# Optimization experiments

Measured on AMD Instinct MI355X. Metric: run time of the kernel, lower is better.

Reference implementation:

```python
import jax, jax.numpy as jnp
import numpy as np

SIGMA_POS = 0.5
SIGMA_FEAT = 1.0


def setup_inputs() -> dict:
    key = jax.random.key(0)
    ks = jax.random.split(key, 6)
    B, N, M, D, F = 4, 4096, 4096, 3, 64
    return {
        "pos1": jax.random.normal(ks[0], (B, N, D), dtype=jnp.float32),
        "feat1": jax.random.normal(ks[1], (B, N, F), dtype=jnp.float32),
        "w1": jax.random.uniform(ks[2], (B, N, 1), dtype=jnp.float32),
        "pos2": jax.random.normal(ks[3], (B, M, D), dtype=jnp.float32),
        "feat2": jax.random.normal(ks[4], (B, M, F), dtype=jnp.float32),
        "w2": jax.random.uniform(ks[5], (B, M, 1), dtype=jnp.float32),
    }


def reference(pos1, feat1, w1, pos2, feat2, w2):
    # pairwise squared distances via |a|^2 + |b|^2 - 2 a.b  (avoids B,N,M,D tensor)
    sq1 = jnp.sum(pos1 ** 2, axis=-1)  # (B, N)
    sq2 = jnp.sum(pos2 ** 2, axis=-1)  # (B, M)
    cross = jnp.einsum("bnd,bmd->bnm", pos1, pos2)  # (B, N, M)
    pos_dist_sq = sq1[:, :, None] + sq2[:, None, :] - 2.0 * cross
    pos_kernel = jnp.exp(-pos_dist_sq / (2.0 * SIGMA_POS ** 2))
    feat_inner = jnp.einsum("bnf,bmf->bnm", feat1, feat2)  # (B, N, M)
    feat_kernel = jnp.exp(-feat_inner / (2.0 * SIGMA_FEAT ** 2))
    weight_outer = w1 * jnp.swapaxes(w2, 1, 2)  # (B,N,1)*(B,1,M) -> (B,N,M)
    kernel = jnp.sum(pos_kernel * feat_kernel * weight_outer, axis=(1, 2))  # (B,)
    return kernel
```

## Files before the change

kernel.cpp:

```cpp
#include <hip/hip_runtime.h>
#include <stdint.h>


typedef _Float16 f16;
typedef _Float16 v8h __attribute__((ext_vector_type(8)));
typedef _Float16 h4  __attribute__((ext_vector_type(4)));
typedef float    v4f __attribute__((ext_vector_type(4)));

#define L2E 1.4426950408889634f
#define BN 4096
#define KP 96

__device__ __forceinline__ void load_lds16(const void* g, void* s) {
    __builtin_amdgcn_global_load_lds((const __attribute__((address_space(1))) void*)g,
                                     (__attribute__((address_space(3))) void*)s,
                                     16, 0, 0);
}

__global__ __launch_bounds__(256) void prep_kernel(
    const float* __restrict__ pos1, const float* __restrict__ feat1, const float* __restrict__ w1,
    const float* __restrict__ pos2, const float* __restrict__ feat2, const float* __restrict__ w2,
    f16* __restrict__ U1, f16* __restrict__ U2,
    float* __restrict__ la1, float* __restrict__ la2)
{
    int tid  = threadIdx.x;
    int ridx = blockIdx.x * 16 + (tid >> 4);
    int c    = tid & 15;
    int side = ridx >> 14;
    int idx  = ridx & 16383;

    const float* feat = side ? feat2 : feat1;
    f16* U   = side ? U2 : U1;
    float fs = side ? -0.5f * L2E : 1.0f;

    float4 v = ((const float4*)feat)[idx * 16 + c];
    *(h4*)(U + (long)idx * KP + 4 + c * 4) =
        h4{(f16)(v.x * fs), (f16)(v.y * fs), (f16)(v.z * fs), (f16)(v.w * fs)};

    if (c == 0) {
        const float* pos = side ? pos2 : pos1;
        const float* w   = side ? w2   : w1;
        float* la = side ? la2 : la1;
        float ps  = side ? 2.0f * L2E : 2.0f;
        float p0 = pos[idx*3+0], p1 = pos[idx*3+1], p2 = pos[idx*3+2];
        la[idx] = __builtin_amdgcn_logf(w[idx]) - 2.0f * L2E * (p0*p0 + p1*p1 + p2*p2);
        *(h4*)(U + (long)idx * KP) = h4{(f16)(p0*ps), (f16)(p1*ps), (f16)(p2*ps), (f16)0.0f};
    } else if (c <= 7) {
        *(h4*)(U + (long)idx * KP + 68 + (c - 1) * 4) =
            h4{(f16)0.0f, (f16)0.0f, (f16)0.0f, (f16)0.0f};
    }
}

__global__ __launch_bounds__(512, 4) void varifold_kernel(
    const f16* __restrict__ U1, const f16* __restrict__ U2,
    const float* __restrict__ la1, const float* __restrict__ la2,
    float* __restrict__ pw)
{
    __shared__ __align__(1024) f16 sAB[(128 + 256) * KP];
    __shared__ float s1[128];
    __shared__ float s2[256];
    __shared__ float sred[8];

    f16* sA = sAB;
    f16* sB = sAB + 128 * KP;

    int mb = blockIdx.x, nb = blockIdx.y, b = blockIdx.z;
    int tid = threadIdx.x;
    int wave = tid >> 6, lane = tid & 63;

    const char* gA = (const char*)(U1 + ((long)b*BN + nb*128) * KP);
    const char* gB = (const char*)(U2 + ((long)b*BN + mb*256) * KP);

    #pragma unroll
    for (int i = 0; i < 9; ++i) {
        int c = wave * 9 + i;
        const char* src = (c < 24) ? (gA + c * 1024 + lane * 16)
                                   : (gB + (c - 24) * 1024 + lane * 16);
        load_lds16(src, (char*)sAB + c * 1024);
    }
    if (tid < 128)      s1[tid]       = la1[(long)b*BN + nb*128 + tid];
    else if (tid < 384) s2[tid - 128] = la2[(long)b*BN + mb*256 + (tid - 128)];
    __syncthreads();

    int wr = wave >> 2, wc = wave & 3;
    int l15 = lane & 15, quad = lane >> 4;
    int ko = quad * 8;

    v4f acc[4][4];
    #pragma unroll
    for (int i = 0; i < 4; ++i)
        #pragma unroll
        for (int j = 0; j < 4; ++j)
            acc[i][j] = v4f{0.f, 0.f, 0.f, 0.f};

    const f16* Ab = sA + (wr*64 + l15) * KP + ko;
    const f16* Bb = sB + (wc*64 + l15) * KP + ko;
    #pragma unroll
    for (int kk = 0; kk < KP; kk += 32) {
        v8h af[4], bf[4];
        #pragma unroll
        for (int i = 0; i < 4; ++i) af[i] = *(const v8h*)(Ab + i*16*KP + kk);
        #pragma unroll
        for (int j = 0; j < 4; ++j) bf[j] = *(const v8h*)(Bb + j*16*KP + kk);
        #pragma unroll
        for (int i = 0; i < 4; ++i)
            #pragma unroll
            for (int j = 0; j < 4; ++j)
                acc[i][j] = __builtin_amdgcn_mfma_f32_16x16x32_f16(af[i], bf[j], acc[i][j], 0, 0, 0);
    }

    float psum = 0.f;
    #pragma unroll
    for (int i = 0; i < 4; ++i) {
        float4 l1 = *(const float4*)&s1[wr*64 + i*16 + quad*4];
        #pragma unroll
        for (int j = 0; j < 4; ++j) {
            float l2 = s2[wc*64 + j*16 + l15];
            v4f d = acc[i][j];
            psum += __builtin_amdgcn_exp2f(d[0] + l1.x + l2);
            psum += __builtin_amdgcn_exp2f(d[1] + l1.y + l2);
            psum += __builtin_amdgcn_exp2f(d[2] + l1.z + l2);
            psum += __builtin_amdgcn_exp2f(d[3] + l1.w + l2);
        }
    }

    #pragma unroll
    for (int off = 32; off > 0; off >>= 1) psum += __shfl_down(psum, off);
    if (lane == 0) sred[wave] = psum;
    __syncthreads();
    if (tid == 0) {
        float s = 0.f;
        #pragma unroll
        for (int w = 0; w < 8; ++w) s += sred[w];
        pw[(long)b * 512 + nb * 16 + mb] = s;
    }
}

__global__ __launch_bounds__(256) void reduce_kernel(
    const float* __restrict__ pw, float* __restrict__ out)
{
    __shared__ float sred[4];
    int b = blockIdx.x, tid = threadIdx.x;
    float v = pw[(long)b * 512 + tid] + pw[(long)b * 512 + 256 + tid];
    #pragma unroll
    for (int off = 32; off > 0; off >>= 1) v += __shfl_down(v, off);
    if ((tid & 63) == 0) sred[tid >> 6] = v;
    __syncthreads();
    if (tid == 0) out[b] = sred[0] + sred[1] + sred[2] + sred[3];
}

extern "C" void kernel_launch(void* const* d_in, const int* in_sizes, int n_in,
                              void* d_out, int out_size, void* d_ws, size_t ws_size,
                              hipStream_t stream) {
    const float* pos1  = (const float*)d_in[0];
    const float* feat1 = (const float*)d_in[1];
    const float* w1    = (const float*)d_in[2];
    const float* pos2  = (const float*)d_in[3];
    const float* feat2 = (const float*)d_in[4];
    const float* w2    = (const float*)d_in[5];
    float* out = (float*)d_out;

    char* ws = (char*)d_ws;
    f16*   U1  = (f16*)(ws);
    f16*   U2  = (f16*)(ws + 3145728);
    float* la1 = (float*)(ws + 6291456);
    float* la2 = (float*)(ws + 6291456 + 65536);
    float* pw  = (float*)(ws + 6291456 + 131072);

    prep_kernel<<<2048, 256, 0, stream>>>(pos1, feat1, w1, pos2, feat2, w2, U1, U2, la1, la2);
    dim3 grid(16, 32, 4);
    varifold_kernel<<<grid, 512, 0, stream>>>(U1, U2, la1, la2, pw);
    reduce_kernel<<<4, 256, 0, stream>>>(pw, out);
}
```

Baseline: 94.04 us.

## Replace LDS-tiled GEMM with register-resident B columns and streamed A rows

Drops the shared-memory staging of both tiles. Each wave now keeps its 64 B columns (all K) in registers and streams 16-row A fragments straight from global memory with a one-step prefetch. It loops over 256 rows per block, so the grid and partial-sum layout change and reduce_kernel sums 1024 partials. This removes the LDS loads, the barrier and the 16-accumulator tile, at the cost of repeated global/L2 reads of A across the waves and stripes and less reuse per loaded fragment.

```diff
diff --git a/kernel.cpp b/kernel.cpp
--- a/kernel.cpp
+++ b/kernel.cpp
@@ -10,12 +10,6 @@
 #define L2E 1.4426950408889634f
 #define BN 4096
 #define KP 96
-
-__device__ __forceinline__ void load_lds16(const void* g, void* s) {
-    __builtin_amdgcn_global_load_lds((const __attribute__((address_space(1))) void*)g,
-                                     (__attribute__((address_space(3))) void*)s,
-                                     16, 0, 0);
-}
 
 __global__ __launch_bounds__(256) void prep_kernel(
     const float* __restrict__ pos1, const float* __restrict__ feat1, const float* __restrict__ w1,
@@ -51,89 +45,69 @@
     }
 }
 
-__global__ __launch_bounds__(512, 4) void varifold_kernel(
+__global__ __launch_bounds__(256, 4) void varifold_kernel(
     const f16* __restrict__ U1, const f16* __restrict__ U2,
     const float* __restrict__ la1, const float* __restrict__ la2,
     float* __restrict__ pw)
 {
-    __shared__ __align__(1024) f16 sAB[(128 + 256) * KP];
-    __shared__ float s1[128];
-    __shared__ float s2[256];
-    __shared__ float sred[8];
+    int tid = threadIdx.x, wave = tid >> 6, lane = tid & 63;
+    int stripe = blockIdx.x, nchunk = blockIdx.y, b = blockIdx.z;
+    int l15 = lane & 15, quad = lane >> 4;
 
-    f16* sA = sAB;
-    f16* sB = sAB + 128 * KP;
+    long colr = (long)b*BN + stripe*256 + wave*64;
+    long row0 = (long)b*BN + nchunk*256;
 
-    int mb = blockIdx.x, nb = blockIdx.y, b = blockIdx.z;
-    int tid = threadIdx.x;
-    int wave = tid >> 6, lane = tid & 63;
+    v8h bf[3][4];
+    float la2v[4];
+    #pragma unroll
+    for (int j = 0; j < 4; ++j) {
+        const f16* r = U2 + (colr + j*16 + l15) * KP + quad*8;
+        bf[0][j] = *(const v8h*)(r);
+        bf[1][j] = *(const v8h*)(r + 32);
+        bf[2][j] = *(const v8h*)(r + 64);
+        la2v[j]  = la2[colr + j*16 + l15];
+    }
 
-    const char* gA = (const char*)(U1 + ((long)b*BN + nb*128) * KP);
-    const char* gB = (const char*)(U2 + ((long)b*BN + mb*256) * KP);
+    const f16* Ab = U1 + (row0 + l15) * KP + quad*8;
+    v8h afc[3], afn[3];
+    afc[0] = *(const v8h*)(Ab);
+    afc[1] = *(const v8h*)(Ab + 32);
+    afc[2] = *(const v8h*)(Ab + 64);
 
-    #pragma unroll
-    for (int i = 0; i < 9; ++i) {
-        int c = wave * 9 + i;
-        const char* src = (c < 24) ? (gA + c * 1024 + lane * 16)
-                                   : (gB + (c - 24) * 1024 + lane * 16);
-        load_lds16(src, (char*)sAB + c * 1024);
-    }
-    if (tid < 128)      s1[tid]       = la1[(long)b*BN + nb*128 + tid];
-    else if (tid < 384) s2[tid - 128] = la2[(long)b*BN + mb*256 + (tid - 128)];
-    __syncthreads();
+    float psum = 0.f;
+    #pragma unroll 2
+    for (int t = 0; t < 16; ++t) {
+        const f16* An = Ab + (t < 15 ? (t+1) : t) * 16 * KP;
+        afn[0] = *(const v8h*)(An);
+        afn[1] = *(const v8h*)(An + 32);
+        afn[2] = *(const v8h*)(An + 64);
 
-    int wr = wave >> 2, wc = wave & 3;
-    int l15 = lane & 15, quad = lane >> 4;
-    int ko = quad * 8;
-
-    v4f acc[4][4];
-    #pragma unroll
-    for (int i = 0; i < 4; ++i)
+        v4f acc[4];
         #pragma unroll
-        for (int j = 0; j < 4; ++j)
-            acc[i][j] = v4f{0.f, 0.f, 0.f, 0.f};
-
-    const f16* Ab = sA + (wr*64 + l15) * KP + ko;
-    const f16* Bb = sB + (wc*64 + l15) * KP + ko;
-    #pragma unroll
-    for (int kk = 0; kk < KP; kk += 32) {
-        v8h af[4], bf[4];
+        for (int j = 0; j < 4; ++j) acc[j] = v4f{0.f, 0.f, 0.f, 0.f};
         #pragma unroll
-        for (int i = 0; i < 4; ++i) af[i] = *(const v8h*)(Ab + i*16*KP + kk);
-        #pragma unroll
-        for (int j = 0; j < 4; ++j) bf[j] = *(const v8h*)(Bb + j*16*KP + kk);
-        #pragma unroll
-        for (int i = 0; i < 4; ++i)
+        for (int k = 0; k < 3; ++k)
             #pragma unroll
             for (int j = 0; j < 4; ++j)
-                acc[i][j] = __builtin_amdgcn_mfma_f32_16x16x32_f16(af[i], bf[j], acc[i][j], 0, 0, 0);
-    }
+                acc[j] = __builtin_amdgcn_mfma_f32_16x16x32_f16(afc[k], bf[k][j], acc[j], 0, 0, 0);
 
-    float psum = 0.f;
-    #pragma unroll
-    for (int i = 0; i < 4; ++i) {
-        float4 l1 = *(const float4*)&s1[wr*64 + i*16 + quad*4];
+        float4 l1 = *(const float4*)(la1 + row0 + t*16 + quad*4);
         #pragma unroll
         for (int j = 0; j < 4; ++j) {
-            float l2 = s2[wc*64 + j*16 + l15];
-            v4f d = acc[i][j];
-            psum += __builtin_amdgcn_exp2f(d[0] + l1.x + l2);
-            psum += __builtin_amdgcn_exp2f(d[1] + l1.y + l2);
-            psum += __builtin_amdgcn_exp2f(d[2] + l1.z + l2);
-            psum += __builtin_amdgcn_exp2f(d[3] + l1.w + l2);
+            v4f d = acc[j];
+            psum += __builtin_amdgcn_exp2f(d[0] + l1.x + la2v[j]);
+            psum += __builtin_amdgcn_exp2f(d[1] + l1.y + la2v[j]);
+            psum += __builtin_amdgcn_exp2f(d[2] + l1.z + la2v[j]);
+            psum += __builtin_amdgcn_exp2f(d[3] + l1.w + la2v[j]);
         }
+
+        afc[0] = afn[0]; afc[1] = afn[1]; afc[2] = afn[2];
     }
 
     #pragma unroll
     for (int off = 32; off > 0; off >>= 1) psum += __shfl_down(psum, off);
-    if (lane == 0) sred[wave] = psum;
-    __syncthreads();
-    if (tid == 0) {
-        float s = 0.f;
-        #pragma unroll
-        for (int w = 0; w < 8; ++w) s += sred[w];
-        pw[(long)b * 512 + nb * 16 + mb] = s;
-    }
+    if (lane == 0)
+        pw[(((long)b*16 + nchunk)*16 + stripe)*4 + wave] = psum;
 }
 
 __global__ __launch_bounds__(256) void reduce_kernel(
@@ -141,7 +115,8 @@
 {
     __shared__ float sred[4];
     int b = blockIdx.x, tid = threadIdx.x;
-    float v = pw[(long)b * 512 + tid] + pw[(long)b * 512 + 256 + tid];
+    const float* p = pw + (long)b * 1024;
+    float v = p[tid] + p[tid + 256] + p[tid + 512] + p[tid + 768];
     #pragma unroll
     for (int off = 32; off > 0; off >>= 1) v += __shfl_down(v, off);
     if ((tid & 63) == 0) sred[tid >> 6] = v;
@@ -168,7 +143,7 @@
     float* pw  = (float*)(ws + 6291456 + 131072);
 
     prep_kernel<<<2048, 256, 0, stream>>>(pos1, feat1, w1, pos2, feat2, w2, U1, U2, la1, la2);
-    dim3 grid(16, 32, 4);
-    varifold_kernel<<<grid, 512, 0, stream>>>(U1, U2, la1, la2, pw);
+    dim3 grid(16, 16, 4);
+    varifold_kernel<<<grid, 256, 0, stream>>>(U1, U2, la1, la2, pw);
     reduce_kernel<<<4, 256, 0, stream>>>(pw, out);
 }
```

Result: no change. 92.95 us (-1.2%).
